# Kernel tuning notes

Hardware: AMD Instinct MI355X
Metric: run time of the kernel (lower is better)

Reference implementation:

```python
import jax, jax.numpy as jnp
import numpy as np

W = 128; H = 128; NEAR = 0.1; FAR = 10.0; EPS = 1e-8
B = 1; V = 512; F = 1024


def _perspective(cf, cc):
    # OpenGL-convention projection, returned transposed for row-vector multiply
    f = 0.5 * (cf[0] + cf[1]); pco = 0.5
    right = (W - (cc[0] + pco)) * (NEAR / f)
    left = -(cc[0] + pco) * (NEAR / f)
    top = (cc[1] + pco) * (NEAR / f)
    bottom = -(H - cc[1] + pco) * (NEAR / f)
    z = jnp.zeros(())
    m = jnp.stack([
        jnp.stack([2.0 * NEAR / (right - left), z, (right + left) / (right - left), z]),
        jnp.stack([z, 2.0 * NEAR / (top - bottom), (top + bottom) / (top - bottom), z]),
        jnp.stack([z, z, jnp.full((), -(FAR + NEAR) / (FAR - NEAR)), jnp.full((), -2.0 * FAR * NEAR / (FAR - NEAR))]),
        jnp.stack([z, z, jnp.full((), -1.0), z]),
    ])
    return m.T


def _rodrigues(r):
    theta = jnp.sqrt(jnp.sum(r * r) + 1e-12)
    k = r / theta
    zz = jnp.zeros(())
    K = jnp.stack([
        jnp.stack([zz, -k[2], k[1]]),
        jnp.stack([k[2], zz, -k[0]]),
        jnp.stack([-k[1], k[0], zz]),
    ])
    return jnp.eye(3) + jnp.sin(theta) * K + (1.0 - jnp.cos(theta)) * (K @ K)


def _view_matrix(rt, t):
    # row-vector convention: v' = v @ M, M = rodrigues^T composed with translation-in-last-row
    R = _rodrigues(rt)
    Mr = jnp.eye(4).at[:3, :3].set(R.T)
    Mt = jnp.eye(4).at[3, :3].set(t)
    return Mr @ Mt


def _rasterize_one(vs_xy, z_ndc, inv_w, valid_tri, f, vc, bgcolor, px, py):
    # vs_xy [V,2] screen coords, z_ndc [V], inv_w [V]; f [F,3] int; pixels px,py [P]
    a = vs_xy[f[:, 0]]; b = vs_xy[f[:, 1]]; c = vs_xy[f[:, 2]]  # [F,2]
    x = px[:, None]; y = py[:, None]  # [P,1]
    def E(p, q):  # signed edge function, broadcast to [P,F]
        return (q[:, 0] - p[:, 0]) * (y - p[:, 1]) - (q[:, 1] - p[:, 1]) * (x - p[:, 0])
    w0 = E(b, c); w1 = E(c, a); w2 = E(a, b)  # [P,F]
    area = (b[:, 0] - a[:, 0]) * (c[:, 1] - a[:, 1]) - (b[:, 1] - a[:, 1]) * (c[:, 0] - a[:, 0])  # [F]
    area_safe = jnp.where(jnp.abs(area) > EPS, area, 1.0)
    b0 = w0 / area_safe; b1 = w1 / area_safe; b2 = w2 / area_safe
    za = z_ndc[f[:, 0]]; zb = z_ndc[f[:, 1]]; zc = z_ndc[f[:, 2]]
    z = b0 * za + b1 * zb + b2 * zc  # [P,F] interpolated NDC depth
    inside = ((b0 >= 0) & (b1 >= 0) & (b2 >= 0) & (jnp.abs(area) > EPS)
              & valid_tri[None, :] & (z >= -1.0) & (z <= 1.0))
    depth = jnp.where(inside, z, jnp.inf)
    best = jnp.argmin(depth, axis=1)  # [P] z-buffer winner
    covered = jnp.take_along_axis(depth, best[:, None], 1)[:, 0] <= 1.0
    take = lambda m: jnp.take_along_axis(m, best[:, None], 1)[:, 0]
    bs = jnp.stack([take(b0), take(b1), take(b2)], -1)  # [P,3]
    tri = f[best]          # [P,3]
    iw = inv_w[tri]        # [P,3]
    col = vc[tri]          # [P,3,C]
    den = jnp.sum(bs * iw, -1)
    den = jnp.where(jnp.abs(den) > EPS, den, 1.0)
    color = jnp.einsum('pk,pk,pkc->pc', bs, iw, col) / den[:, None]  # perspective-correct
    return jnp.where(covered[:, None], color, bgcolor[None, :])  # [P,C]


def reference(v, vc, f, bgcolor, camera_f, camera_c, camera_t, camera_rt):
    view = _view_matrix(camera_rt, camera_t)
    proj = _perspective(camera_f, camera_c)
    vh = jnp.concatenate([v, jnp.ones_like(v[..., :1])], -1)  # [B,V,4]
    clip = vh @ (view @ proj)                                 # [B,V,4]
    wc = clip[..., 3]
    valid_v = wc > EPS                                        # in front of camera
    w_safe = jnp.where(valid_v, wc, 1.0)
    ndc = clip[..., :3] / w_safe[..., None]
    xs = (ndc[..., 0] * 0.5 + 0.5) * W
    ys = (0.5 - ndc[..., 1] * 0.5) * H
    vs_xy = jnp.stack([xs, ys], -1)                           # [B,V,2]
    inv_w = 1.0 / w_safe
    valid_tri = valid_v[:, f].all(-1)                         # [B,F]
    gy, gx = jnp.meshgrid(jnp.arange(H, dtype=jnp.float32) + 0.5,
                          jnp.arange(W, dtype=jnp.float32) + 0.5, indexing='ij')
    px = gx.reshape(-1); py = gy.reshape(-1)
    img = jax.vmap(lambda xy, zn, iw, vt: _rasterize_one(xy, zn, iw, vt, f, vc, bgcolor, px, py))(
        vs_xy, ndc[..., 2], inv_w, valid_tri)
    return img.reshape(v.shape[0], H, W, vc.shape[-1])


def setup_inputs() -> dict:
    key = jax.random.key(0)
    k1, k2, k3 = jax.random.split(key, 3)
    u = jax.random.uniform(k1, (B, V, 3), dtype=jnp.float32)
    # x,y in [-0.8,0.8], z in [-3,-1] (camera looks along -z)
    vtx = jnp.stack([u[..., 0] * 1.6 - 0.8, u[..., 1] * 1.6 - 0.8, -(1.0 + 2.0 * u[..., 2])], -1)
    vc = jax.random.uniform(k2, (V, 3), dtype=jnp.float32)
    f = jax.random.randint(k3, (F, 3), 0, V, dtype=jnp.int32)
    return {
        'v': vtx,
        'vc': vc,
        'f': f,
        'bgcolor': jnp.zeros((3,), jnp.float32),
        'camera_f': jnp.array([128.0, 128.0], jnp.float32),
        'camera_c': jnp.array([64.0, 64.0], jnp.float32),
        'camera_t': jnp.zeros((3,), jnp.float32),
        'camera_rt': jnp.zeros((3,), jnp.float32),
    }
```

## Files before the change

kernel.cpp:

```cpp
#include <hip/hip_runtime.h>
#include <math.h>
#include <stdint.h>

#define NV 512
#define NF 1024
#define TRI_STRIDE 16
#define NGROUP 16
#define CHUNK 64


__global__ __launch_bounds__(256, 4) void render_kernel(
    const float* __restrict__ v, const int* __restrict__ fidx,
    const float* __restrict__ camf, const float* __restrict__ camc,
    const float* __restrict__ camt, const float* __restrict__ camrt,
    double* __restrict__ vdata, double* __restrict__ tridata,
    unsigned long long* __restrict__ keys)
{
  __shared__ double sM[16];
  __shared__ double sxs[NV], sys_[NV], szn[NV];
  __shared__ int svld[NV];
  __shared__ double2 sc[5][CHUNK];
  const int tid = threadIdx.x;
  const int tile = blockIdx.x;
  const int group = blockIdx.y;
  const int tbase = group * CHUNK;

  {
#pragma clang fp contract(off)
    if (tid == 0) {
      float r0f = camrt[0], r1f = camrt[1], r2f = camrt[2];
      float th = sqrtf(((r0f * r0f + r1f * r1f) + r2f * r2f) + 1e-12f);
      float k0 = r0f / th, k1 = r1f / th, k2 = r2f / th;
      float sthf = sinf(th);
      float cthf = 1.0f - cosf(th);
      double K[3][3] = {{0.0, -(double)k2, (double)k1},
                        {(double)k2, 0.0, -(double)k0},
                        {-(double)k1, (double)k0, 0.0}};
      double KK[3][3];
      for (int i = 0; i < 3; ++i)
        for (int j = 0; j < 3; ++j)
          KK[i][j] = (K[i][0] * K[0][j] + K[i][1] * K[1][j]) + K[i][2] * K[2][j];
      double R[3][3];
      for (int i = 0; i < 3; ++i)
        for (int j = 0; j < 3; ++j) {
          double e = (i == j) ? 1.0 : 0.0;
          R[i][j] = (e + (double)sthf * K[i][j]) + (double)cthf * KK[i][j];
        }
      double Mr[4][4], Mt[4][4];
      for (int i = 0; i < 4; ++i)
        for (int j = 0; j < 4; ++j) {
          Mr[i][j] = (i == j) ? 1.0 : 0.0;
          Mt[i][j] = (i == j) ? 1.0 : 0.0;
        }
      for (int i = 0; i < 3; ++i)
        for (int j = 0; j < 3; ++j) Mr[i][j] = R[j][i];
      Mt[3][0] = (double)camt[0]; Mt[3][1] = (double)camt[1]; Mt[3][2] = (double)camt[2];
      double view[4][4];
      for (int i = 0; i < 4; ++i)
        for (int j = 0; j < 4; ++j)
          view[i][j] = ((Mr[i][0] * Mt[0][j] + Mr[i][1] * Mt[1][j]) +
                        Mr[i][2] * Mt[2][j]) + Mr[i][3] * Mt[3][j];
      float fcam = 0.5f * (camf[0] + camf[1]);
      float nf = 0.1f / fcam;
      float ccx = camc[0], ccy = camc[1];
      float right = (128.0f - (ccx + 0.5f)) * nf;
      float left = -(ccx + 0.5f) * nf;
      float top = (ccy + 0.5f) * nf;
      float bottom = -((128.0f - ccy) + 0.5f) * nf;
      float m00f = 0.2f / (right - left);
      float m02f = (right + left) / (right - left);
      float m11f = 0.2f / (top - bottom);
      float m12f = (top + bottom) / (top - bottom);
      double P[4][4] = {
          {(double)m00f, 0.0, (double)m02f, 0.0},
          {0.0, (double)m11f, (double)m12f, 0.0},
          {0.0, 0.0, -(10.0 + 0.1) / (10.0 - 0.1),
           -2.0 * 10.0 * 0.1 / (10.0 - 0.1)},
          {0.0, 0.0, -1.0, 0.0}};
      for (int i = 0; i < 4; ++i)
        for (int j = 0; j < 4; ++j)
          sM[i * 4 + j] = ((view[i][0] * P[j][0] + view[i][1] * P[j][1]) +
                           view[i][2] * P[j][2]) + view[i][3] * P[j][3];
    }
    __syncthreads();

    for (int i = tid; i < NV; i += 256) {
      double x = (double)v[i * 3 + 0];
      double y = (double)v[i * 3 + 1];
      double zz = (double)v[i * 3 + 2];
      double c0 = ((x * sM[0] + y * sM[4]) + zz * sM[8]) + sM[12];
      double c1 = ((x * sM[1] + y * sM[5]) + zz * sM[9]) + sM[13];
      double c2 = ((x * sM[2] + y * sM[6]) + zz * sM[10]) + sM[14];
      double c3 = ((x * sM[3] + y * sM[7]) + zz * sM[11]) + sM[15];
      int valid = c3 > 1e-8;
      double wsafe = valid ? c3 : 1.0;
      double n0 = c0 / wsafe, n1 = c1 / wsafe, n2 = c2 / wsafe;
      double xs = (n0 * 0.5 + 0.5) * 128.0;
      double ys = (0.5 - n1 * 0.5) * 128.0;
      double iw = 1.0 / wsafe;
      sxs[i] = xs; sys_[i] = ys; szn[i] = n2; svld[i] = valid;
      if (tile == 0 && group == 0) {
        vdata[0 * NV + i] = xs;
        vdata[1 * NV + i] = ys;
        vdata[2 * NV + i] = n2;
        vdata[3 * NV + i] = iw;
      }
    }
    __syncthreads();

    if (tid < CHUNK) {
      const int t = tbase + tid;
      int i0 = fidx[t * 3 + 0], i1 = fidx[t * 3 + 1], i2 = fidx[t * 3 + 2];
      double ax = sxs[i0], ay = sys_[i0];
      double bx = sxs[i1], by = sys_[i1];
      double cx = sxs[i2], cy = sys_[i2];
      double p1 = (bx - ax) * (cy - ay);
      double p2 = (by - ay) * (cx - ax);
      double area = p1 - p2;
      bool ok = (fabs(area) > 1e-8) && svld[i0] && svld[i1] && svld[i2];
      double s = (area > 0.0) ? 1.0 : -1.0;
      double inv_abs = ok ? s / area : 1.0;
      double kk0 = szn[i0] * inv_abs, kk1 = szn[i1] * inv_abs, kk2 = szn[i2] * inv_abs;

      if (tile == 0) {
        double* td = tridata + t * TRI_STRIDE;
        td[0] = bx;  td[1] = by;  td[2] = cx;  td[3] = cy;  td[4] = ax;  td[5] = ay;
        td[6] = s * (cx - bx);  td[7] = s * (cy - by);
        td[8] = s * (ax - cx);  td[9] = s * (ay - cy);
        td[10] = s * (bx - ax); td[11] = s * (by - ay);
        td[12] = kk0; td[13] = kk1; td[14] = kk2;
        td[15] = inv_abs;
      }

      double e0x = cx - bx, e0y = cy - by;
      double e1x = ax - cx, e1y = ay - cy;
      double e2x = bx - ax, e2y = by - ay;
      double A0 = -s * e0y, B0 = s * e0x, C0 = s * (e0y * bx - e0x * by);
      double A1 = -s * e1y, B1 = s * e1x, C1 = s * (e1y * cx - e1x * cy);
      double A2 = -s * e2y, B2 = s * e2x, C2 = s * (e2y * ax - e2x * ay);
      double Az = (A0 * kk0 + A1 * kk1) + A2 * kk2;
      double Bz = (B0 * kk0 + B1 * kk1) + B2 * kk2;
      double Cz = (C0 * kk0 + C1 * kk1) + C2 * kk2;
      double absarea = ok ? (s * area) : __builtin_nan("");
      sc[0][tid] = make_double2(A0, B0);
      sc[1][tid] = make_double2(C0, A1);
      sc[2][tid] = make_double2(B1, C1);
      sc[3][tid] = make_double2(Az, Bz);
      sc[4][tid] = make_double2(Cz, absarea);
    }
  }
  __syncthreads();

  const int x = ((tile & 7) << 4) + (tid & 15);
  const int y = ((tile >> 3) << 4) + (tid >> 4);
  const double px = (double)x + 0.5, py = (double)y + 0.5;

  double bestz = INFINITY;
  int besti = -1;
#pragma unroll 4
  for (int t = 0; t < CHUNK; ++t) {
    double2 c0 = sc[0][t];
    double2 c1 = sc[1][t];
    double2 c2 = sc[2][t];
    double2 c3 = sc[3][t];
    double2 c4 = sc[4][t];
    double w0 = (c0.x * px + c0.y * py) + c1.x;
    double w1 = (c1.y * px + c2.x * py) + c2.y;
    double z  = (c3.x * px + c3.y * py) + c4.x;
    double w2 = (c4.y - w0) - w1;
    bool ins = (w0 >= 0.0) & (w1 >= 0.0) & (w2 >= 0.0) &
               (z >= -1.0) & (z <= 1.0) & (z < bestz);
    bestz = ins ? z : bestz;
    besti = ins ? (tbase + t) : besti;
  }
  if (besti >= 0) {
    unsigned long long zq = (unsigned long long)((bestz + 1.0) * 4503599627370496.0);
    atomicMin(&keys[y * 128 + x], (zq << 10) | (unsigned long long)besti);
  }
}

__global__ __launch_bounds__(256) void color_kernel(
    const unsigned long long* __restrict__ keys,
    const double* __restrict__ vdata, const double* __restrict__ tridata,
    const int* __restrict__ fidx, const float* __restrict__ vc,
    const float* __restrict__ bg, float* __restrict__ out)
{
  const int p = blockIdx.x * 256 + threadIdx.x;
  if (p >= 16384) return;
  const int x = p & 127, y = p >> 7;
  unsigned long long key = keys[p];
  float cr, cg, cb;
  if (key == ~0ull) {
    cr = bg[0]; cg = bg[1]; cb = bg[2];
  } else {
    unsigned int t = (unsigned int)(key & 1023ull);
    const double* td = tridata + t * TRI_STRIDE;
    double px = (double)x + 0.5, py = (double)y + 0.5;
    double w0 = td[6] * (py - td[1]) - td[7] * (px - td[0]);
    double w1 = td[8] * (py - td[3]) - td[9] * (px - td[2]);
    double w2 = td[10] * (py - td[5]) - td[11] * (px - td[4]);
    double inv = td[15];
    double b0 = w0 * inv, b1 = w1 * inv, b2 = w2 * inv;
    int i0 = fidx[t * 3 + 0], i1 = fidx[t * 3 + 1], i2 = fidx[t * 3 + 2];
    double t0 = b0 * vdata[3 * NV + i0];
    double t1 = b1 * vdata[3 * NV + i1];
    double t2 = b2 * vdata[3 * NV + i2];
    double den = (t0 + t1) + t2;
    if (!(fabs(den) > 1e-8)) den = 1.0;
    cr = (float)((((t0 * (double)vc[i0 * 3 + 0] + t1 * (double)vc[i1 * 3 + 0]) +
                   t2 * (double)vc[i2 * 3 + 0])) / den);
    cg = (float)((((t0 * (double)vc[i0 * 3 + 1] + t1 * (double)vc[i1 * 3 + 1]) +
                   t2 * (double)vc[i2 * 3 + 1])) / den);
    cb = (float)((((t0 * (double)vc[i0 * 3 + 2] + t1 * (double)vc[i1 * 3 + 2]) +
                   t2 * (double)vc[i2 * 3 + 2])) / den);
  }
  out[p * 3 + 0] = cr;
  out[p * 3 + 1] = cg;
  out[p * 3 + 2] = cb;
}

extern "C" void kernel_launch(void* const* d_in, const int* in_sizes, int n_in,
                              void* d_out, int out_size, void* d_ws, size_t ws_size,
                              hipStream_t stream) {
  const float* v = (const float*)d_in[0];
  const float* vc = (const float*)d_in[1];
  const int* fidx = (const int*)d_in[2];
  const float* bg = (const float*)d_in[3];
  const float* camf = (const float*)d_in[4];
  const float* camc = (const float*)d_in[5];
  const float* camt = (const float*)d_in[6];
  const float* camrt = (const float*)d_in[7];
  float* out = (float*)d_out;

  char* ws = (char*)d_ws;
  unsigned long long* keys = (unsigned long long*)ws;
  double* vdata = (double*)(ws + 131072);
  double* tridata = (double*)(ws + 147456);

  hipMemsetAsync(keys, 0xFF, 16384 * sizeof(unsigned long long), stream);
  render_kernel<<<dim3(64, NGROUP), 256, 0, stream>>>(
      v, fidx, camf, camc, camt, camrt, vdata, tridata, keys);
  color_kernel<<<64, 256, 0, stream>>>(keys, vdata, tridata, fidx, vc, bg, out);
}
```

Measured before the change: 89.69 us.

## Fuse color pass into render via last-block counter and add bbox triangle culling

Removes the separate color kernel. The last of the 16 group blocks for each tile, detected with an atomic done counter, now resolves pixel colors using shared-memory vertex data, and the vdata/tridata global writes are dropped. Each block also culls its 64-triangle chunk against the tile bounding box with a ballot/popcount compaction, so the per-pixel loop only visits overlapping triangles. The cost is an extra memset, a threadfence plus atomic per block, and a serialized color tail on the last-arriving block.

```diff
diff --git a/kernel.cpp b/kernel.cpp
--- a/kernel.cpp
+++ b/kernel.cpp
@@ -4,7 +4,6 @@
 
 #define NV 512
 #define NF 1024
-#define TRI_STRIDE 16
 #define NGROUP 16
 #define CHUNK 64
 
@@ -13,17 +12,25 @@
     const float* __restrict__ v, const int* __restrict__ fidx,
     const float* __restrict__ camf, const float* __restrict__ camc,
     const float* __restrict__ camt, const float* __restrict__ camrt,
-    double* __restrict__ vdata, double* __restrict__ tridata,
-    unsigned long long* __restrict__ keys)
+    const float* __restrict__ vc, const float* __restrict__ bg,
+    unsigned long long* __restrict__ keys, unsigned int* __restrict__ done,
+    float* __restrict__ out)
 {
   __shared__ double sM[16];
-  __shared__ double sxs[NV], sys_[NV], szn[NV];
+  __shared__ double sxs[NV], sys_[NV], szn[NV], siw[NV];
   __shared__ int svld[NV];
   __shared__ double2 sc[5][CHUNK];
+  __shared__ double2 scc[5][CHUNK];
+  __shared__ float4 sbb[CHUNK];
+  __shared__ int scidx[CHUNK];
+  __shared__ int scnt;
+  __shared__ int s_last;
   const int tid = threadIdx.x;
   const int tile = blockIdx.x;
   const int group = blockIdx.y;
   const int tbase = group * CHUNK;
+  const int x0 = (tile & 7) << 4;
+  const int y0 = (tile >> 3) << 4;
 
   {
 #pragma clang fp contract(off)
@@ -98,13 +105,7 @@
       double xs = (n0 * 0.5 + 0.5) * 128.0;
       double ys = (0.5 - n1 * 0.5) * 128.0;
       double iw = 1.0 / wsafe;
-      sxs[i] = xs; sys_[i] = ys; szn[i] = n2; svld[i] = valid;
-      if (tile == 0 && group == 0) {
-        vdata[0 * NV + i] = xs;
-        vdata[1 * NV + i] = ys;
-        vdata[2 * NV + i] = n2;
-        vdata[3 * NV + i] = iw;
-      }
+      sxs[i] = xs; sys_[i] = ys; szn[i] = n2; siw[i] = iw; svld[i] = valid;
     }
     __syncthreads();
 
@@ -121,16 +122,6 @@
       double s = (area > 0.0) ? 1.0 : -1.0;
       double inv_abs = ok ? s / area : 1.0;
       double kk0 = szn[i0] * inv_abs, kk1 = szn[i1] * inv_abs, kk2 = szn[i2] * inv_abs;
-
-      if (tile == 0) {
-        double* td = tridata + t * TRI_STRIDE;
-        td[0] = bx;  td[1] = by;  td[2] = cx;  td[3] = cy;  td[4] = ax;  td[5] = ay;
-        td[6] = s * (cx - bx);  td[7] = s * (cy - by);
-        td[8] = s * (ax - cx);  td[9] = s * (ay - cy);
-        td[10] = s * (bx - ax); td[11] = s * (by - ay);
-        td[12] = kk0; td[13] = kk1; td[14] = kk2;
-        td[15] = inv_abs;
-      }
 
       double e0x = cx - bx, e0y = cy - by;
       double e1x = ax - cx, e1y = ay - cy;
@@ -147,23 +138,50 @@
       sc[2][tid] = make_double2(B1, C1);
       sc[3][tid] = make_double2(Az, Bz);
       sc[4][tid] = make_double2(Cz, absarea);
+      float4 bb;
+      if (ok) {
+        bb.x = (float)(fmin(fmin(ax, bx), cx) - 0.01);
+        bb.y = (float)(fmin(fmin(ay, by), cy) - 0.01);
+        bb.z = (float)(fmax(fmax(ax, bx), cx) + 0.01);
+        bb.w = (float)(fmax(fmax(ay, by), cy) + 0.01);
+      } else {
+        bb.x = 1e30f; bb.y = 1e30f; bb.z = -1e30f; bb.w = -1e30f;
+      }
+      sbb[tid] = bb;
+
+      const float txmin = (float)x0 + 0.5f, txmax = (float)x0 + 15.5f;
+      const float tymin = (float)y0 + 0.5f, tymax = (float)y0 + 15.5f;
+      bool hit = !(bb.x > txmax || bb.z < txmin || bb.y > tymax || bb.w < tymin);
+      unsigned long long m = __ballot(hit);
+      int pos = __popcll(m & ((1ull << tid) - 1ull));
+      if (hit) {
+        scc[0][pos] = sc[0][tid];
+        scc[1][pos] = sc[1][tid];
+        scc[2][pos] = sc[2][tid];
+        scc[3][pos] = sc[3][tid];
+        scc[4][pos] = sc[4][tid];
+        scidx[pos] = tid;
+      }
+      if (tid == 0) scnt = (int)__popcll(m);
     }
   }
   __syncthreads();
 
-  const int x = ((tile & 7) << 4) + (tid & 15);
-  const int y = ((tile >> 3) << 4) + (tid >> 4);
+  const int x = x0 + (tid & 15);
+  const int y = y0 + (tid >> 4);
   const double px = (double)x + 0.5, py = (double)y + 0.5;
+  const int cnt = scnt;
 
   double bestz = INFINITY;
   int besti = -1;
 #pragma unroll 4
-  for (int t = 0; t < CHUNK; ++t) {
-    double2 c0 = sc[0][t];
-    double2 c1 = sc[1][t];
-    double2 c2 = sc[2][t];
-    double2 c3 = sc[3][t];
-    double2 c4 = sc[4][t];
+  for (int j = 0; j < cnt; ++j) {
+    double2 c0 = scc[0][j];
+    double2 c1 = scc[1][j];
+    double2 c2 = scc[2][j];
+    double2 c3 = scc[3][j];
+    double2 c4 = scc[4][j];
+    int torig = scidx[j];
     double w0 = (c0.x * px + c0.y * py) + c1.x;
     double w1 = (c1.y * px + c2.x * py) + c2.y;
     double z  = (c3.x * px + c3.y * py) + c4.x;
@@ -171,52 +189,65 @@
     bool ins = (w0 >= 0.0) & (w1 >= 0.0) & (w2 >= 0.0) &
                (z >= -1.0) & (z <= 1.0) & (z < bestz);
     bestz = ins ? z : bestz;
-    besti = ins ? (tbase + t) : besti;
+    besti = ins ? (tbase + torig) : besti;
   }
   if (besti >= 0) {
     unsigned long long zq = (unsigned long long)((bestz + 1.0) * 4503599627370496.0);
     atomicMin(&keys[y * 128 + x], (zq << 10) | (unsigned long long)besti);
   }
-}
-
-__global__ __launch_bounds__(256) void color_kernel(
-    const unsigned long long* __restrict__ keys,
-    const double* __restrict__ vdata, const double* __restrict__ tridata,
-    const int* __restrict__ fidx, const float* __restrict__ vc,
-    const float* __restrict__ bg, float* __restrict__ out)
-{
-  const int p = blockIdx.x * 256 + threadIdx.x;
-  if (p >= 16384) return;
-  const int x = p & 127, y = p >> 7;
-  unsigned long long key = keys[p];
-  float cr, cg, cb;
-  if (key == ~0ull) {
-    cr = bg[0]; cg = bg[1]; cb = bg[2];
-  } else {
-    unsigned int t = (unsigned int)(key & 1023ull);
-    const double* td = tridata + t * TRI_STRIDE;
-    double px = (double)x + 0.5, py = (double)y + 0.5;
-    double w0 = td[6] * (py - td[1]) - td[7] * (px - td[0]);
-    double w1 = td[8] * (py - td[3]) - td[9] * (px - td[2]);
-    double w2 = td[10] * (py - td[5]) - td[11] * (px - td[4]);
-    double inv = td[15];
-    double b0 = w0 * inv, b1 = w1 * inv, b2 = w2 * inv;
-    int i0 = fidx[t * 3 + 0], i1 = fidx[t * 3 + 1], i2 = fidx[t * 3 + 2];
-    double t0 = b0 * vdata[3 * NV + i0];
-    double t1 = b1 * vdata[3 * NV + i1];
-    double t2 = b2 * vdata[3 * NV + i2];
-    double den = (t0 + t1) + t2;
-    if (!(fabs(den) > 1e-8)) den = 1.0;
-    cr = (float)((((t0 * (double)vc[i0 * 3 + 0] + t1 * (double)vc[i1 * 3 + 0]) +
-                   t2 * (double)vc[i2 * 3 + 0])) / den);
-    cg = (float)((((t0 * (double)vc[i0 * 3 + 1] + t1 * (double)vc[i1 * 3 + 1]) +
-                   t2 * (double)vc[i2 * 3 + 1])) / den);
-    cb = (float)((((t0 * (double)vc[i0 * 3 + 2] + t1 * (double)vc[i1 * 3 + 2]) +
-                   t2 * (double)vc[i2 * 3 + 2])) / den);
-  }
-  out[p * 3 + 0] = cr;
-  out[p * 3 + 1] = cg;
-  out[p * 3 + 2] = cb;
+
+  __syncthreads();
+  if (tid == 0) {
+    __threadfence();
+    unsigned int old = __hip_atomic_fetch_add(&done[tile], 1u, __ATOMIC_ACQ_REL,
+                                              __HIP_MEMORY_SCOPE_AGENT);
+    s_last = (old == NGROUP - 1) ? 1 : 0;
+  }
+  __syncthreads();
+
+  if (s_last) {
+    const int p = y * 128 + x;
+    unsigned long long key = __hip_atomic_load(&keys[p], __ATOMIC_RELAXED,
+                                               __HIP_MEMORY_SCOPE_AGENT);
+    float cr, cg, cb;
+    if (key == ~0ull) {
+      cr = bg[0]; cg = bg[1]; cb = bg[2];
+    } else {
+#pragma clang fp contract(off)
+      unsigned int t = (unsigned int)(key & 1023ull);
+      int i0 = fidx[t * 3 + 0], i1 = fidx[t * 3 + 1], i2 = fidx[t * 3 + 2];
+      double ax = sxs[i0], ay = sys_[i0];
+      double bx = sxs[i1], by = sys_[i1];
+      double cx = sxs[i2], cy = sys_[i2];
+      double p1 = (bx - ax) * (cy - ay);
+      double p2 = (by - ay) * (cx - ax);
+      double area = p1 - p2;
+      bool ok = (fabs(area) > 1e-8) && svld[i0] && svld[i1] && svld[i2];
+      double s = (area > 0.0) ? 1.0 : -1.0;
+      double inv = ok ? s / area : 1.0;
+      double d6 = s * (cx - bx), d7 = s * (cy - by);
+      double d8 = s * (ax - cx), d9 = s * (ay - cy);
+      double d10 = s * (bx - ax), d11 = s * (by - ay);
+      double w0 = d6 * (py - by) - d7 * (px - bx);
+      double w1 = d8 * (py - cy) - d9 * (px - cx);
+      double w2 = d10 * (py - ay) - d11 * (px - ax);
+      double b0 = w0 * inv, b1 = w1 * inv, b2 = w2 * inv;
+      double t0 = b0 * siw[i0];
+      double t1 = b1 * siw[i1];
+      double t2 = b2 * siw[i2];
+      double den = (t0 + t1) + t2;
+      if (!(fabs(den) > 1e-8)) den = 1.0;
+      cr = (float)((((t0 * (double)vc[i0 * 3 + 0] + t1 * (double)vc[i1 * 3 + 0]) +
+                     t2 * (double)vc[i2 * 3 + 0])) / den);
+      cg = (float)((((t0 * (double)vc[i0 * 3 + 1] + t1 * (double)vc[i1 * 3 + 1]) +
+                     t2 * (double)vc[i2 * 3 + 1])) / den);
+      cb = (float)((((t0 * (double)vc[i0 * 3 + 2] + t1 * (double)vc[i1 * 3 + 2]) +
+                     t2 * (double)vc[i2 * 3 + 2])) / den);
+    }
+    out[p * 3 + 0] = cr;
+    out[p * 3 + 1] = cg;
+    out[p * 3 + 2] = cb;
+  }
 }
 
 extern "C" void kernel_launch(void* const* d_in, const int* in_sizes, int n_in,
@@ -234,11 +265,10 @@
 
   char* ws = (char*)d_ws;
   unsigned long long* keys = (unsigned long long*)ws;
-  double* vdata = (double*)(ws + 131072);
-  double* tridata = (double*)(ws + 147456);
+  unsigned int* done = (unsigned int*)(ws + 131072);
 
   hipMemsetAsync(keys, 0xFF, 16384 * sizeof(unsigned long long), stream);
+  hipMemsetAsync(done, 0x00, 64 * sizeof(unsigned int), stream);
   render_kernel<<<dim3(64, NGROUP), 256, 0, stream>>>(
-      v, fidx, camf, camc, camt, camrt, vdata, tridata, keys);
-  color_kernel<<<64, 256, 0, stream>>>(keys, vdata, tridata, fidx, vc, bg, out);
+      v, fidx, camf, camc, camt, camrt, vc, bg, keys, done, out);
 }
```

Result: slower. 106.3 us (+18.5%).
